# Performance work log

Hardware: AMD Instinct MI355X
Metric: run time of the kernel (lower is better)

## Reference

```python
import jax, jax.numpy as jnp
import numpy as np

B, N, D, DN, F, NUM_F, O, H = 8, 4096, 256, 128, 128, 1024, 8, 1024
EPS = 1e-5

def setup_inputs() -> dict:
    key = jax.random.key(0)
    ks = jax.random.split(key, 10)
    s = 0.02
    x = jax.random.normal(ks[0], (B, N, D), dtype=jnp.float32)
    ctx = jax.random.normal(ks[1], (B, DN), dtype=jnp.float32)
    idx = jax.random.randint(ks[2], (F,), 0, NUM_F, dtype=jnp.int64)
    cond_w = jax.random.normal(ks[3], (DN, 2 * D), dtype=jnp.float32) * s
    cond_b = jnp.zeros((2 * D,), dtype=jnp.float32)
    ffn_w_in = jax.random.normal(ks[4], (D, 2 * H), dtype=jnp.float32) * s
    ffn_b_in = jnp.zeros((2 * H,), dtype=jnp.float32)
    ffn_w_out = jax.random.normal(ks[5], (H, D), dtype=jnp.float32) * s
    ffn_b_out = jnp.zeros((D,), dtype=jnp.float32)
    emb = jax.random.normal(ks[6], (NUM_F, D * O), dtype=jnp.float32) * s
    return {"x": x, "ctx": ctx, "idx": idx, "cond_w": cond_w, "cond_b": cond_b,
            "ffn_w_in": ffn_w_in, "ffn_b_in": ffn_b_in,
            "ffn_w_out": ffn_w_out, "ffn_b_out": ffn_b_out, "emb": emb}

def reference(x, ctx, idx, cond_w, cond_b, ffn_w_in, ffn_b_in, ffn_w_out, ffn_b_out, emb):
    # Conditional LayerNorm: normalize over last dim, FiLM-style modulation from ctx
    mu = jnp.mean(x, axis=-1, keepdims=True)
    var = jnp.mean((x - mu) ** 2, axis=-1, keepdims=True)
    h = (x - mu) * jax.lax.rsqrt(var + EPS)                      # [B,N,D]
    ss = ctx @ cond_w + cond_b                                   # [B,2D]
    scale, shift = jnp.split(ss, 2, axis=-1)                     # [B,D] each
    h = h * (1.0 + scale[:, None, :]) + shift[:, None, :]
    # Gated FFN: in-proj -> (gelu(gate) * value) -> out-proj
    uv = h @ ffn_w_in + ffn_b_in                                 # [B,N,2H]
    u, v = jnp.split(uv, 2, axis=-1)
    y = (jax.nn.gelu(u) * v) @ ffn_w_out + ffn_b_out             # [B,N,D]
    # Embedding-generated per-feature output weights, then batched contraction
    w = emb[idx].reshape(F, D, O)                                # gather [F,D,O]
    out = jnp.einsum('bnd,fdo->bnfo', y, w)                      # [B,N,F,O]
    return out
```

## Files before the change

kernel.cpp:

```cpp
#include <hip/hip_runtime.h>
#include <cstdint>
#include <cstddef>

#define M_TOT 32768
#define D_    256
#define DN_   128
#define TWO_D 512
#define H_    1024
#define TWO_H 2048

typedef unsigned short ushort_t;
typedef __attribute__((ext_vector_type(8))) short bf16x8;
typedef __attribute__((ext_vector_type(4))) float f32x4;

__device__ __forceinline__ ushort_t f2bf(float f) {
  union { float f; uint32_t i; } v; v.f = f;
  uint32_t r = v.i + 0x7fffu + ((v.i >> 16) & 1u);
  return (ushort_t)(r >> 16);
}

__device__ __forceinline__ void async_ld16(const void* g, void* l) {
  __builtin_amdgcn_global_load_lds(
      (const __attribute__((address_space(1))) void*)g,
      (__attribute__((address_space(3))) void*)l, 16, 0, 0);
}

__global__ __launch_bounds__(256) void cond_ss_kernel(
    const float* __restrict__ ctx, const float* __restrict__ cond_w,
    const float* __restrict__ cond_b, float* __restrict__ ss) {
  int j = blockIdx.x * 256 + threadIdx.x;
  int b = j >> 9, col = j & 511;
  float acc = cond_b[col];
  for (int k = 0; k < DN_; ++k)
    acc += ctx[b * DN_ + k] * cond_w[k * TWO_D + col];
  ss[j] = acc;
}

__global__ __launch_bounds__(256) void transpose_f32_bf16_kernel(
    const float* __restrict__ in, ushort_t* __restrict__ out, int R, int C) {
  __shared__ float T[64 * 65];
  int ctiles = C >> 6;
  int bi = blockIdx.x / ctiles, bj = blockIdx.x % ctiles;
  int r0 = bi * 64, c0 = bj * 64;
  int tid = threadIdx.x;
#pragma unroll
  for (int it = 0; it < 16; ++it) {
    int idx = it * 256 + tid;
    int r = idx >> 6, c = idx & 63;
    T[r * 65 + c] = in[(size_t)(r0 + r) * C + c0 + c];
  }
  __syncthreads();
#pragma unroll
  for (int it = 0; it < 8; ++it) {
    int idx = it * 256 + tid;
    int a = idx >> 5;
    int b = (idx & 31) * 2;
    uint32_t pk = (uint32_t)f2bf(T[b * 65 + a]) |
                  ((uint32_t)f2bf(T[(b + 1) * 65 + a]) << 16);
    *(uint32_t*)&out[(size_t)(c0 + a) * R + r0 + b] = pk;
  }
}

__global__ __launch_bounds__(256) void gather_emb_kernel(
    const float* __restrict__ emb, const int* __restrict__ idx,
    ushort_t* __restrict__ W2T) {
  int f = blockIdx.x;
  bool looks64 = (idx[1] == 0) & (idx[3] == 0) & (idx[5] == 0) & (idx[7] == 0);
  int fi = looks64 ? idx[2 * f] : idx[f];
  const float* src = emb + (size_t)fi * 2048;
  int o = threadIdx.x >> 5, d0 = (threadIdx.x & 31) * 8;
  ushort_t buf[8];
#pragma unroll
  for (int k = 0; k < 8; ++k) buf[k] = f2bf(src[(d0 + k) * 8 + o]);
  *(bf16x8*)&W2T[(size_t)(f * 8 + o) * 256 + d0] = *(bf16x8*)buf;
}

__global__ __launch_bounds__(256) void ln_film_kernel(
    const float* __restrict__ x, const float* __restrict__ ss,
    ushort_t* __restrict__ h) {
  int row = blockIdx.x * 4 + (threadIdx.x >> 6);
  int lane = threadIdx.x & 63;
  int b = row >> 12;
  const float* xr = x + (size_t)row * D_;
  float4 pk = *(const float4*)(xr + lane * 4);
  float f0 = pk.x, f1 = pk.y, f2 = pk.z, f3 = pk.w;
  float s = f0 + f1 + f2 + f3;
  float q = f0 * f0 + f1 * f1 + f2 * f2 + f3 * f3;
#pragma unroll
  for (int off = 32; off > 0; off >>= 1) {
    s += __shfl_xor(s, off, 64);
    q += __shfl_xor(q, off, 64);
  }
  float mean = s * (1.0f / 256.0f);
  float var = q * (1.0f / 256.0f) - mean * mean;
  float rs = rsqrtf(var + 1e-5f);
  int d = lane * 4;
  const float* ssb = ss + b * TWO_D;
  float o0 = (f0 - mean) * rs * (1.0f + ssb[d + 0]) + ssb[256 + d + 0];
  float o1 = (f1 - mean) * rs * (1.0f + ssb[d + 1]) + ssb[256 + d + 1];
  float o2 = (f2 - mean) * rs * (1.0f + ssb[d + 2]) + ssb[256 + d + 2];
  float o3 = (f3 - mean) * rs * (1.0f + ssb[d + 3]) + ssb[256 + d + 3];
  uint2 st;
  st.x = (uint32_t)f2bf(o0) | ((uint32_t)f2bf(o1) << 16);
  st.y = (uint32_t)f2bf(o2) | ((uint32_t)f2bf(o3) << 16);
  *(uint2*)(h + (size_t)row * D_ + lane * 4) = st;
}

__global__ __launch_bounds__(512, 2) void ffn_fused_kernel(
    const ushort_t* __restrict__ h,
    const ushort_t* __restrict__ WinT,
    const float* __restrict__ bin,
    const ushort_t* __restrict__ WoutT,
    const float* __restrict__ bout,
    ushort_t* __restrict__ y) {
  __shared__ ushort_t S3[3][8192];
  __shared__ ushort_t Gs[128 * 72];
  __shared__ float Lbin[2048];
  const int tid = threadIdx.x, lane = tid & 63, wave = tid >> 6;
  const int wm = wave >> 1, wn = wave & 1;
  const int r = lane >> 2, q = lane & 3;
  const int qs = q ^ ((r >> 1) & 3);
  const int l15 = lane & 15, l4 = lane >> 4;
  const int m0 = blockIdx.x * 128;
  const int fragoff = l15 * 32 + (l4 ^ ((l15 >> 1) & 3)) * 8;

  const char* winb  = (const char*)WinT  + r * 512 + qs * 16;
  const char* woutb = (const char*)WoutT + r * 2048 + qs * 16;

  const ushort_t* hp = h + (size_t)(m0 + wm * 32 + l15) * 256 + l4 * 8;
  bf16x8 a_reg[2][8];
#pragma unroll
  for (int rt = 0; rt < 2; ++rt)
#pragma unroll
    for (int kc = 0; kc < 8; ++kc)
      a_reg[rt][kc] = *(const bf16x8*)(hp + rt * 4096 + kc * 32);

  async_ld16((const char*)bin + wave * 1024 + lane * 16,
             (char*)Lbin + wave * 1024);

  auto stage_in = [&](ushort_t* dst, int jrow, int k0e) {
#pragma unroll
    for (int i = 0; i < 2; ++i) {
      int tt = i * 8 + wave;
      int vv = tt >> 3, t7 = tt & 7;
      int ks = t7 >> 2, cc = t7 & 3;
      async_ld16(winb + (size_t)vv * 524288 + jrow * 32768 + cc * 8192 +
                     k0e * 2 + ks * 64,
                 &dst[tt * 512]);
    }
  };
  auto stage_wout = [&](ushort_t* dst, int jrow, int s2) {
#pragma unroll
    for (int i = 0; i < 2; ++i) {
      int tt = i * 8 + wave;
      async_ld16(woutb + (size_t)tt * 32768 + jrow * 128 + s2 * 64,
                 &dst[tt * 512]);
    }
  };

  stage_in(S3[0], 0, 0);
  stage_in(S3[1], 0, 64);

  f32x4 yac[2][8] = {};

#define ENTRY2()                                        \
  asm volatile("s_waitcnt vmcnt(2)" ::: "memory");      \
  __builtin_amdgcn_s_barrier();                         \
  asm volatile("" ::: "memory");
#define ENTRY2L()                                                  \
  asm volatile("s_waitcnt vmcnt(2) lgkmcnt(0)" ::: "memory");      \
  __builtin_amdgcn_s_barrier();                                    \
  asm volatile("" ::: "memory");

#define MFMA_IN(buf, p_)                                                      \
  {                                                                           \
    const ushort_t* cur_ = (buf);                                             \
    __builtin_amdgcn_s_setprio(1);                                            \
    _Pragma("unroll")                                                         \
    for (int ks = 0; ks < 2; ++ks) {                                          \
      _Pragma("unroll")                                                       \
      for (int jj = 0; jj < 2; ++jj) {                                        \
        int tt = ks * 4 + wn * 2 + jj;                                        \
        bf16x8 bu = *(const bf16x8*)&cur_[tt * 512 + fragoff];                \
        bf16x8 bv = *(const bf16x8*)&cur_[(8 + tt) * 512 + fragoff];          \
        uac[0][jj] = __builtin_amdgcn_mfma_f32_16x16x32_bf16(a_reg[0][(p_)*2+ks], bu, uac[0][jj], 0, 0, 0); \
        uac[1][jj] = __builtin_amdgcn_mfma_f32_16x16x32_bf16(a_reg[1][(p_)*2+ks], bu, uac[1][jj], 0, 0, 0); \
        vac[0][jj] = __builtin_amdgcn_mfma_f32_16x16x32_bf16(a_reg[0][(p_)*2+ks], bv, vac[0][jj], 0, 0, 0); \
        vac[1][jj] = __builtin_amdgcn_mfma_f32_16x16x32_bf16(a_reg[1][(p_)*2+ks], bv, vac[1][jj], 0, 0, 0); \
      }                                                                       \
    }                                                                         \
    __builtin_amdgcn_s_setprio(0);                                            \
  }

#define MFMA_OUT(buf, s2_)                                                    \
  {                                                                           \
    const ushort_t* cur_ = (buf);                                             \
    bf16x8 gf0 = *(const bf16x8*)&Gs[(wm * 32 + l15) * 72 + (s2_) * 32 + l4 * 8];      \
    bf16x8 gf1 = *(const bf16x8*)&Gs[(wm * 32 + 16 + l15) * 72 + (s2_) * 32 + l4 * 8]; \
    __builtin_amdgcn_s_setprio(1);                                            \
    _Pragma("unroll")                                                         \
    for (int nt8 = 0; nt8 < 8; ++nt8) {                                       \
      bf16x8 bw = *(const bf16x8*)&cur_[(wn * 8 + nt8) * 512 + fragoff];      \
      yac[0][nt8] = __builtin_amdgcn_mfma_f32_16x16x32_bf16(gf0, bw, yac[0][nt8], 0, 0, 0); \
      yac[1][nt8] = __builtin_amdgcn_mfma_f32_16x16x32_bf16(gf1, bw, yac[1][nt8], 0, 0, 0); \
    }                                                                         \
    __builtin_amdgcn_s_setprio(0);                                            \
  }

  for (int j = 0; j < 16; ++j) {
    const int jn = (j + 1) & 15;
    f32x4 uac[2][2] = {}, vac[2][2] = {};

    ENTRY2(); stage_in(S3[2], j, 128);  MFMA_IN(S3[0], 0);
    ENTRY2(); stage_in(S3[0], j, 192);  MFMA_IN(S3[1], 1);
    ENTRY2(); stage_wout(S3[1], j, 0);  MFMA_IN(S3[2], 2);
    ENTRY2(); stage_wout(S3[2], j, 1);  MFMA_IN(S3[0], 3);

#pragma unroll
    for (int jj = 0; jj < 2; ++jj) {
      int gcol = wn * 32 + jj * 16 + l15;
      float bub = Lbin[j * 64 + gcol];
      float bvb = Lbin[1024 + j * 64 + gcol];
#pragma unroll
      for (int rt = 0; rt < 2; ++rt) {
#pragma unroll
        for (int rr = 0; rr < 4; ++rr) {
          float u = uac[rt][jj][rr] + bub;
          float v = vac[rt][jj][rr] + bvb;
          float t = 0.7978845608028654f * (u + 0.044715f * u * u * u);
          float e = __expf(2.0f * t);
          float th = 1.0f - 2.0f / (e + 1.0f);
          float gl = 0.5f * u * (1.0f + th);
          Gs[(wm * 32 + rt * 16 + l4 * 4 + rr) * 72 + gcol] = f2bf(gl * v);
        }
      }
    }

    ENTRY2L(); stage_in(S3[0], jn, 0);  MFMA_OUT(S3[1], 0);
    ENTRY2();  stage_in(S3[1], jn, 64); MFMA_OUT(S3[2], 1);
  }

  asm volatile("s_waitcnt vmcnt(0)" ::: "memory");
  __builtin_amdgcn_s_barrier();
  asm volatile("" ::: "memory");
  ushort_t* E = &S3[0][0];
#pragma unroll
  for (int hh = 0; hh < 2; ++hh) {
    if ((wm >> 1) == hh) {
      int er0 = (wm & 1) * 32;
#pragma unroll
      for (int nt8 = 0; nt8 < 8; ++nt8) {
        int col = wn * 128 + nt8 * 16 + l15;
        float bb = bout[col];
#pragma unroll
        for (int rt = 0; rt < 2; ++rt)
#pragma unroll
          for (int rr = 0; rr < 4; ++rr)
            E[(er0 + rt * 16 + l4 * 4 + rr) * 264 + col] = f2bf(yac[rt][nt8][rr] + bb);
      }
    }
    asm volatile("s_waitcnt lgkmcnt(0)" ::: "memory");
    __builtin_amdgcn_s_barrier();
    asm volatile("" ::: "memory");
#pragma unroll
    for (int it = 0; it < 4; ++it) {
      int id = it * 512 + tid;
      int rr = id >> 5, cc = id & 31;
      bf16x8 vv = *(const bf16x8*)&E[rr * 264 + cc * 8];
      *(bf16x8*)&y[(size_t)(m0 + hh * 64 + rr) * 256 + cc * 8] = vv;
    }
    if (hh == 0) {
      __builtin_amdgcn_s_barrier();
      asm volatile("" ::: "memory");
    }
  }
#undef ENTRY2
#undef ENTRY2L
#undef MFMA_IN
#undef MFMA_OUT
}

__global__ __launch_bounds__(256, 2) void gemm_out_kernel(
    const ushort_t* __restrict__ A, const ushort_t* __restrict__ BT,
    float* __restrict__ C) {
  __shared__ ushort_t SB[2][16384];
  const int tid = threadIdx.x, lane = tid & 63, wave = tid >> 6;
  const int wm = wave >> 1, wn = wave & 1;
  const int m0 = blockIdx.x * 128, n0 = blockIdx.y * 128;
  const int r = lane >> 2, q = lane & 3;
  const int qs = q ^ ((r >> 1) & 3);
  const int l15 = lane & 15, l4 = lane >> 4;
  const int fragoff = l15 * 32 + (l4 ^ ((l15 >> 1) & 3)) * 8;
  const int N = 1024, K = 256;

  auto stage = [&](ushort_t* dst, int k0) {
#pragma unroll
    for (int i = 0; i < 4; ++i) {
      int t = i * 4 + wave;
      int rt = t >> 1, ks = t & 1;
      async_ld16(A + (size_t)(m0 + rt * 16 + r) * K + k0 + ks * 32 + qs * 8, &dst[t * 512]);
      async_ld16(BT + (size_t)(n0 + rt * 16 + r) * K + k0 + ks * 32 + qs * 8, &dst[(16 + t) * 512]);
    }
  };

  f32x4 acc[4][4] = {};
  stage(SB[0], 0);
#pragma unroll
  for (int ki = 0; ki < 4; ++ki) {
    __builtin_amdgcn_s_barrier();
    asm volatile("" ::: "memory");
    if (ki < 3) {
      stage(SB[(ki + 1) & 1], (ki + 1) * 64);
      asm volatile("s_waitcnt vmcnt(8)" ::: "memory");
    } else {
      asm volatile("s_waitcnt vmcnt(0)" ::: "memory");
    }
    __builtin_amdgcn_s_barrier();
    asm volatile("" ::: "memory");
    const ushort_t* cur = SB[ki & 1];
    __builtin_amdgcn_s_setprio(1);
#pragma unroll
    for (int ks = 0; ks < 2; ++ks) {
      bf16x8 a[4], b[4];
#pragma unroll
      for (int i = 0; i < 4; ++i)
        a[i] = *(const bf16x8*)&cur[((wm * 4 + i) * 2 + ks) * 512 + fragoff];
#pragma unroll
      for (int jt = 0; jt < 4; ++jt)
        b[jt] = *(const bf16x8*)&cur[(16 + (wn * 4 + jt) * 2 + ks) * 512 + fragoff];
#pragma unroll
      for (int i = 0; i < 4; ++i)
#pragma unroll
        for (int jt = 0; jt < 4; ++jt)
          acc[i][jt] = __builtin_amdgcn_mfma_f32_16x16x32_bf16(a[i], b[jt], acc[i][jt], 0, 0, 0);
    }
    __builtin_amdgcn_s_setprio(0);
  }
#pragma unroll
  for (int jt = 0; jt < 4; ++jt) {
    int col = n0 + wn * 64 + jt * 16 + l15;
#pragma unroll
    for (int i = 0; i < 4; ++i) {
      int row = m0 + wm * 64 + i * 16 + l4 * 4;
#pragma unroll
      for (int rr = 0; rr < 4; ++rr)
        C[(size_t)(row + rr) * N + col] = acc[i][jt][rr];
    }
  }
}

extern "C" void kernel_launch(void* const* d_in, const int* in_sizes, int n_in,
                              void* d_out, int out_size, void* d_ws, size_t ws_size,
                              hipStream_t stream) {
  const float* x      = (const float*)d_in[0];
  const float* ctx    = (const float*)d_in[1];
  const int*   idx    = (const int*)d_in[2];
  const float* cond_w = (const float*)d_in[3];
  const float* cond_b = (const float*)d_in[4];
  const float* w_in   = (const float*)d_in[5];
  const float* b_in   = (const float*)d_in[6];
  const float* w_out  = (const float*)d_in[7];
  const float* b_out  = (const float*)d_in[8];
  const float* emb    = (const float*)d_in[9];

  char* w = (char*)d_ws;
  float* ss = (float*)w;           w += (size_t)8 * TWO_D * 4;
  ushort_t* h = (ushort_t*)w;      w += (size_t)M_TOT * D_ * 2;
  ushort_t* y = (ushort_t*)w;      w += (size_t)M_TOT * D_ * 2;
  ushort_t* WinT = (ushort_t*)w;   w += (size_t)TWO_H * D_ * 2;
  ushort_t* WoutT = (ushort_t*)w;  w += (size_t)D_ * H_ * 2;
  ushort_t* W2T = (ushort_t*)w;    w += (size_t)H_ * D_ * 2;

  cond_ss_kernel<<<16, 256, 0, stream>>>(ctx, cond_w, cond_b, ss);
  transpose_f32_bf16_kernel<<<(D_ / 64) * (TWO_H / 64), 256, 0, stream>>>(w_in, WinT, D_, TWO_H);
  transpose_f32_bf16_kernel<<<(H_ / 64) * (D_ / 64), 256, 0, stream>>>(w_out, WoutT, H_, D_);
  gather_emb_kernel<<<128, 256, 0, stream>>>(emb, idx, W2T);
  ln_film_kernel<<<M_TOT / 4, 256, 0, stream>>>(x, ss, h);
  ffn_fused_kernel<<<M_TOT / 128, 512, 0, stream>>>(h, WinT, b_in, WoutT, b_out, y);
  gemm_out_kernel<<<dim3(M_TOT / 128, H_ / 128), 256, 0, stream>>>(y, W2T, (float*)d_out);
}
```

Before: 292.9 us.

## Fuse LN-FiLM into FFN, merge prep kernels, stage output stores via LDS

Merges the four small weight-prep kernels into one launch that dispatches on block index. The LayerNorm+FiLM step now runs inside the FFN kernel, which reads fp32 x directly, so the bf16 intermediate h never goes through global memory. The output GEMM epilogue now stages the accumulators in shared memory and writes coalesced float4 rows instead of scattered scalar stores. The trade-off is two extra barriers in the epilogue and extra register pressure from the in-kernel LN, whose x rows are now read twice from global memory.

Measured after the change: 297.8 us. Within noise of the previous version (+1.7%).

```diff
diff --git a/kernel.cpp b/kernel.cpp
--- a/kernel.cpp
+++ b/kernel.cpp
@@ -25,24 +25,12 @@
       (__attribute__((address_space(3))) void*)l, 16, 0, 0);
 }
 
-__global__ __launch_bounds__(256) void cond_ss_kernel(
-    const float* __restrict__ ctx, const float* __restrict__ cond_w,
-    const float* __restrict__ cond_b, float* __restrict__ ss) {
-  int j = blockIdx.x * 256 + threadIdx.x;
-  int b = j >> 9, col = j & 511;
-  float acc = cond_b[col];
-  for (int k = 0; k < DN_; ++k)
-    acc += ctx[b * DN_ + k] * cond_w[k * TWO_D + col];
-  ss[j] = acc;
-}
-
-__global__ __launch_bounds__(256) void transpose_f32_bf16_kernel(
-    const float* __restrict__ in, ushort_t* __restrict__ out, int R, int C) {
-  __shared__ float T[64 * 65];
+__device__ __forceinline__ void transpose_body(
+    const float* __restrict__ in, ushort_t* __restrict__ out, int R, int C,
+    int bb, int tid, float* T) {
   int ctiles = C >> 6;
-  int bi = blockIdx.x / ctiles, bj = blockIdx.x % ctiles;
+  int bi = bb / ctiles, bj = bb % ctiles;
   int r0 = bi * 64, c0 = bj * 64;
-  int tid = threadIdx.x;
 #pragma unroll
   for (int it = 0; it < 16; ++it) {
     int idx = it * 256 + tid;
@@ -61,53 +49,42 @@
   }
 }
 
-__global__ __launch_bounds__(256) void gather_emb_kernel(
+__global__ __launch_bounds__(256) void prep_kernel(
+    const float* __restrict__ ctx, const float* __restrict__ cond_w,
+    const float* __restrict__ cond_b, float* __restrict__ ss,
+    const float* __restrict__ w_in, ushort_t* __restrict__ WinT,
+    const float* __restrict__ w_out, ushort_t* __restrict__ WoutT,
     const float* __restrict__ emb, const int* __restrict__ idx,
     ushort_t* __restrict__ W2T) {
-  int f = blockIdx.x;
-  bool looks64 = (idx[1] == 0) & (idx[3] == 0) & (idx[5] == 0) & (idx[7] == 0);
-  int fi = looks64 ? idx[2 * f] : idx[f];
-  const float* src = emb + (size_t)fi * 2048;
-  int o = threadIdx.x >> 5, d0 = (threadIdx.x & 31) * 8;
-  ushort_t buf[8];
-#pragma unroll
-  for (int k = 0; k < 8; ++k) buf[k] = f2bf(src[(d0 + k) * 8 + o]);
-  *(bf16x8*)&W2T[(size_t)(f * 8 + o) * 256 + d0] = *(bf16x8*)buf;
-}
-
-__global__ __launch_bounds__(256) void ln_film_kernel(
-    const float* __restrict__ x, const float* __restrict__ ss,
-    ushort_t* __restrict__ h) {
-  int row = blockIdx.x * 4 + (threadIdx.x >> 6);
-  int lane = threadIdx.x & 63;
-  int b = row >> 12;
-  const float* xr = x + (size_t)row * D_;
-  float4 pk = *(const float4*)(xr + lane * 4);
-  float f0 = pk.x, f1 = pk.y, f2 = pk.z, f3 = pk.w;
-  float s = f0 + f1 + f2 + f3;
-  float q = f0 * f0 + f1 * f1 + f2 * f2 + f3 * f3;
-#pragma unroll
-  for (int off = 32; off > 0; off >>= 1) {
-    s += __shfl_xor(s, off, 64);
-    q += __shfl_xor(q, off, 64);
-  }
-  float mean = s * (1.0f / 256.0f);
-  float var = q * (1.0f / 256.0f) - mean * mean;
-  float rs = rsqrtf(var + 1e-5f);
-  int d = lane * 4;
-  const float* ssb = ss + b * TWO_D;
-  float o0 = (f0 - mean) * rs * (1.0f + ssb[d + 0]) + ssb[256 + d + 0];
-  float o1 = (f1 - mean) * rs * (1.0f + ssb[d + 1]) + ssb[256 + d + 1];
-  float o2 = (f2 - mean) * rs * (1.0f + ssb[d + 2]) + ssb[256 + d + 2];
-  float o3 = (f3 - mean) * rs * (1.0f + ssb[d + 3]) + ssb[256 + d + 3];
-  uint2 st;
-  st.x = (uint32_t)f2bf(o0) | ((uint32_t)f2bf(o1) << 16);
-  st.y = (uint32_t)f2bf(o2) | ((uint32_t)f2bf(o3) << 16);
-  *(uint2*)(h + (size_t)row * D_ + lane * 4) = st;
+  __shared__ float T[64 * 65];
+  int bid = blockIdx.x, tid = threadIdx.x;
+  if (bid < 16) {
+    int j = bid * 256 + tid;
+    int b = j >> 9, col = j & 511;
+    float acc = cond_b[col];
+    for (int k = 0; k < DN_; ++k)
+      acc += ctx[b * DN_ + k] * cond_w[k * TWO_D + col];
+    ss[j] = acc;
+  } else if (bid < 144) {
+    transpose_body(w_in, WinT, D_, TWO_H, bid - 16, tid, T);
+  } else if (bid < 208) {
+    transpose_body(w_out, WoutT, H_, D_, bid - 144, tid, T);
+  } else {
+    int f = bid - 208;
+    bool looks64 = (idx[1] == 0) & (idx[3] == 0) & (idx[5] == 0) & (idx[7] == 0);
+    int fi = looks64 ? idx[2 * f] : idx[f];
+    const float* src = emb + (size_t)fi * 2048;
+    int o = tid >> 5, d0 = (tid & 31) * 8;
+    ushort_t buf[8];
+#pragma unroll
+    for (int k = 0; k < 8; ++k) buf[k] = f2bf(src[(d0 + k) * 8 + o]);
+    *(bf16x8*)&W2T[(size_t)(f * 8 + o) * 256 + d0] = *(bf16x8*)buf;
+  }
 }
 
 __global__ __launch_bounds__(512, 2) void ffn_fused_kernel(
-    const ushort_t* __restrict__ h,
+    const float* __restrict__ x,
+    const float* __restrict__ ss,
     const ushort_t* __restrict__ WinT,
     const float* __restrict__ bin,
     const ushort_t* __restrict__ WoutT,
@@ -127,13 +104,66 @@
   const char* winb  = (const char*)WinT  + r * 512 + qs * 16;
   const char* woutb = (const char*)WoutT + r * 2048 + qs * 16;
 
-  const ushort_t* hp = h + (size_t)(m0 + wm * 32 + l15) * 256 + l4 * 8;
+  const float* xb = x + (size_t)(m0 + wm * 32 + l15) * 256 + l4 * 8;
+  const float* ssb = ss + (m0 >> 12) * TWO_D + l4 * 8;
   bf16x8 a_reg[2][8];
 #pragma unroll
-  for (int rt = 0; rt < 2; ++rt)
-#pragma unroll
-    for (int kc = 0; kc < 8; ++kc)
-      a_reg[rt][kc] = *(const bf16x8*)(hp + rt * 4096 + kc * 32);
+  for (int rt = 0; rt < 2; ++rt) {
+    const float* xr = xb + rt * 16 * 256;
+    float p[8][2], qq[8][2];
+#pragma unroll
+    for (int kc = 0; kc < 8; ++kc) {
+      float4 u0 = *(const float4*)(xr + kc * 32);
+      float4 u1 = *(const float4*)(xr + kc * 32 + 4);
+      p[kc][0]  = ((u0.x + u0.y) + u0.z) + u0.w;
+      qq[kc][0] = ((u0.x * u0.x + u0.y * u0.y) + u0.z * u0.z) + u0.w * u0.w;
+      p[kc][1]  = ((u1.x + u1.y) + u1.z) + u1.w;
+      qq[kc][1] = ((u1.x * u1.x + u1.y * u1.y) + u1.z * u1.z) + u1.w * u1.w;
+    }
+    float s2[2], q2[2];
+#pragma unroll
+    for (int e = 0; e < 2; ++e) {
+      float a0 = p[0][e] + p[4][e], a1 = p[1][e] + p[5][e];
+      float a2 = p[2][e] + p[6][e], a3 = p[3][e] + p[7][e];
+      float b0 = a0 + a2, b1 = a1 + a3;
+      s2[e] = b0 + b1;
+      float c0 = qq[0][e] + qq[4][e], c1 = qq[1][e] + qq[5][e];
+      float c2 = qq[2][e] + qq[6][e], c3 = qq[3][e] + qq[7][e];
+      float d0 = c0 + c2, d1 = c1 + c3;
+      q2[e] = d0 + d1;
+    }
+#pragma unroll
+    for (int e = 0; e < 2; ++e) {
+      s2[e] += __shfl_xor(s2[e], 32, 64);
+      q2[e] += __shfl_xor(q2[e], 32, 64);
+      s2[e] += __shfl_xor(s2[e], 16, 64);
+      q2[e] += __shfl_xor(q2[e], 16, 64);
+    }
+    float s = s2[0] + s2[1];
+    float qsum = q2[0] + q2[1];
+    float mean = s * (1.0f / 256.0f);
+    float var = qsum * (1.0f / 256.0f) - mean * mean;
+    float rs = rsqrtf(var + 1e-5f);
+#pragma unroll
+    for (int kc = 0; kc < 8; ++kc) {
+      float4 u0 = *(const float4*)(xr + kc * 32);
+      float4 u1 = *(const float4*)(xr + kc * 32 + 4);
+      float4 g0 = *(const float4*)(ssb + kc * 32);
+      float4 g1 = *(const float4*)(ssb + kc * 32 + 4);
+      float4 t0 = *(const float4*)(ssb + 256 + kc * 32);
+      float4 t1 = *(const float4*)(ssb + 256 + kc * 32 + 4);
+      ushort_t hb[8];
+      hb[0] = f2bf((u0.x - mean) * rs * (1.0f + g0.x) + t0.x);
+      hb[1] = f2bf((u0.y - mean) * rs * (1.0f + g0.y) + t0.y);
+      hb[2] = f2bf((u0.z - mean) * rs * (1.0f + g0.z) + t0.z);
+      hb[3] = f2bf((u0.w - mean) * rs * (1.0f + g0.w) + t0.w);
+      hb[4] = f2bf((u1.x - mean) * rs * (1.0f + g1.x) + t1.x);
+      hb[5] = f2bf((u1.y - mean) * rs * (1.0f + g1.y) + t1.y);
+      hb[6] = f2bf((u1.z - mean) * rs * (1.0f + g1.z) + t1.z);
+      hb[7] = f2bf((u1.w - mean) * rs * (1.0f + g1.w) + t1.w);
+      a_reg[rt][kc] = *(bf16x8*)hb;
+    }
+  }
 
   async_ld16((const char*)bin + wave * 1024 + lane * 16,
              (char*)Lbin + wave * 1024);
@@ -336,15 +366,33 @@
     }
     __builtin_amdgcn_s_setprio(0);
   }
-#pragma unroll
-  for (int jt = 0; jt < 4; ++jt) {
-    int col = n0 + wn * 64 + jt * 16 + l15;
-#pragma unroll
-    for (int i = 0; i < 4; ++i) {
-      int row = m0 + wm * 64 + i * 16 + l4 * 4;
-#pragma unroll
-      for (int rr = 0; rr < 4; ++rr)
-        C[(size_t)(row + rr) * N + col] = acc[i][jt][rr];
+  float* Cs = (float*)&SB[0][0];
+#pragma unroll
+  for (int p = 0; p < 2; ++p) {
+    __builtin_amdgcn_s_barrier();
+    asm volatile("" ::: "memory");
+    if (wm == p) {
+#pragma unroll
+      for (int jt = 0; jt < 4; ++jt) {
+        int col = wn * 64 + jt * 16 + l15;
+#pragma unroll
+        for (int i = 0; i < 4; ++i) {
+          int rl = i * 16 + (l4 << 2);
+#pragma unroll
+          for (int rr = 0; rr < 4; ++rr)
+            Cs[(rl + rr) * 132 + col] = acc[i][jt][rr];
+        }
+      }
+    }
+    asm volatile("s_waitcnt lgkmcnt(0)" ::: "memory");
+    __builtin_amdgcn_s_barrier();
+    asm volatile("" ::: "memory");
+#pragma unroll
+    for (int it = 0; it < 8; ++it) {
+      int t = it * 256 + tid;
+      int rr = t >> 5, c = (t & 31) * 4;
+      float4 v = *(const float4*)&Cs[rr * 132 + c];
+      *(float4*)&C[(size_t)(m0 + p * 64 + rr) * N + n0 + c] = v;
     }
   }
 }
@@ -365,17 +413,13 @@
 
   char* w = (char*)d_ws;
   float* ss = (float*)w;           w += (size_t)8 * TWO_D * 4;
-  ushort_t* h = (ushort_t*)w;      w += (size_t)M_TOT * D_ * 2;
   ushort_t* y = (ushort_t*)w;      w += (size_t)M_TOT * D_ * 2;
   ushort_t* WinT = (ushort_t*)w;   w += (size_t)TWO_H * D_ * 2;
   ushort_t* WoutT = (ushort_t*)w;  w += (size_t)D_ * H_ * 2;
   ushort_t* W2T = (ushort_t*)w;    w += (size_t)H_ * D_ * 2;
 
-  cond_ss_kernel<<<16, 256, 0, stream>>>(ctx, cond_w, cond_b, ss);
-  transpose_f32_bf16_kernel<<<(D_ / 64) * (TWO_H / 64), 256, 0, stream>>>(w_in, WinT, D_, TWO_H);
-  transpose_f32_bf16_kernel<<<(H_ / 64) * (D_ / 64), 256, 0, stream>>>(w_out, WoutT, H_, D_);
-  gather_emb_kernel<<<128, 256, 0, stream>>>(emb, idx, W2T);
-  ln_film_kernel<<<M_TOT / 4, 256, 0, stream>>>(x, ss, h);
-  ffn_fused_kernel<<<M_TOT / 128, 512, 0, stream>>>(h, WinT, b_in, WoutT, b_out, y);
+  prep_kernel<<<336, 256, 0, stream>>>(ctx, cond_w, cond_b, ss,
+                                       w_in, WinT, w_out, WoutT, emb, idx, W2T);
+  ffn_fused_kernel<<<M_TOT / 128, 512, 0, stream>>>(x, ss, WinT, b_in, WoutT, b_out, y);
   gemm_out_kernel<<<dim3(M_TOT / 128, H_ / 128), 256, 0, stream>>>(y, W2T, (float*)d_out);
 }
```
